# Kernel tuning notes

Hardware: AMD Instinct MI355X
Metric: run time of the kernel (lower is better)

Reference implementation:

```python
import jax, jax.numpy as jnp
import numpy as np

N_NODES = 50000
N_DIRECTED = 800000  # symmetrized to 1.6M (src,dst) pairs
IN_FEAT = 256
HEADS = 8
OUT = 64


def setup_inputs() -> dict:
    key = jax.random.key(0)
    k1, k2, k3, k4, k5 = jax.random.split(key, 5)
    r = jax.random.randint(k1, (N_DIRECTED,), 0, N_NODES)
    c = jax.random.randint(k2, (N_DIRECTED,), 0, N_NODES)
    # symmetric adjacency (values = 1), as edge list
    src = jnp.concatenate([r, c])
    dst = jnp.concatenate([c, r])
    x = jax.random.normal(k3, (N_NODES, IN_FEAT), dtype=jnp.float32)
    Ws = jax.random.normal(k4, (HEADS, OUT, IN_FEAT), dtype=jnp.float32) * 0.05
    As = jax.random.normal(k5, (HEADS, 2 * OUT, 1), dtype=jnp.float32) * 0.05
    return {"x": x, "src": src, "dst": dst, "Ws": Ws, "As": As}


def reference(x, src, dst, Ws, As):
    H, O, F = Ws.shape
    N = x.shape[0]
    # t_nodes = inputs @ Ws^T  -> [H, N, O]
    t = jnp.einsum('nf,hof->hno', x, Ws)
    a_l = As[:, :O, 0]   # [H, O]
    a_r = As[:, O:, 0]   # [H, O]
    Al = jnp.einsum('hno,ho->hn', t, a_l)  # [H, N]
    Ar = jnp.einsum('hno,ho->hn', t, a_r)  # [H, N]
    outs = []
    for k in range(H):
        # sparse E[i,j] = Al[i] + Ar[j] on adjacency pattern
        e = Al[k][src] + Ar[k][dst]  # [E]
        # NOTE: original applies tf.sparse.softmax to E directly (its lrelu
        # tensor is computed but never used), so no leaky_relu here.
        m = jax.ops.segment_max(e, src, num_segments=N)
        ex = jnp.exp(e - m[src])
        den = jax.ops.segment_sum(ex, src, num_segments=N)
        alpha = ex / den[src]
        # sparse_dense_matmul(alphas, t_nodes[k])
        h = jax.ops.segment_sum(alpha[:, None] * t[k][dst], src, num_segments=N)
        outs.append(h)
    out = jnp.stack(outs, axis=1)          # [N, H, O]
    out = out.reshape(N, H * O)            # reduction=False -> concat heads
    return jax.nn.elu(out)
```

## Files before the change

### kernel.cpp

```cpp
#include <hip/hip_runtime.h>
#include <hip/hip_bf16.h>

#define NN 50000
#define INF 256
#define NH 8
#define OUTF 64
#define NC 512
#define NGB 3128
#define EPB 8192
#define NBK 391
#define NBX 12501

typedef __attribute__((ext_vector_type(8))) short bf16x8;
typedef __attribute__((ext_vector_type(4))) float f32x4;
typedef __attribute__((ext_vector_type(2))) float v2f;
typedef __attribute__((ext_vector_type(8))) float f32x8;

__device__ __forceinline__ unsigned short f2bf(float f){
  unsigned u = __float_as_uint(f);
  u += 0x7FFFu + ((u>>16)&1u);
  return (unsigned short)(u>>16);
}

__global__ void k_atil(const float* __restrict__ W, const float* __restrict__ As,
                       float* __restrict__ atil, int* __restrict__ cursor){
  const int h = blockIdx.x, f = threadIdx.x;
  if (h==0 && f==0){ cursor[0]=0; cursor[1]=0; }
  float s = 0.f;
  for (int o=0;o<64;o++) s += W[((long)h*64+o)*INF + f] * As[h*128 + 64 + o];
  atil[h*256 + f] = s;
}

__global__ __launch_bounds__(256) void k_front(const float* __restrict__ x,
                                               const float* __restrict__ W,
                                               unsigned short* __restrict__ Wt,
                                               const float* __restrict__ atil,
                                               unsigned short* __restrict__ xb,
                                               float* __restrict__ eAr,
                                               const int* __restrict__ src,
                                               int* __restrict__ M,
                                               int E, int NB){
  __shared__ int hh[NBK];
  const int tid = threadIdx.x;
  const int bid = blockIdx.x;
  if (bid < 8){
    const int r = tid>>2, cb = (tid&3)*64;
    char* tile = (char*)(Wt + (size_t)bid*16384);
    const float* Wr = W + ((long)bid*64 + r)*INF;
#pragma unroll
    for (int i=0;i<16;i++){
      int c = cb + i*4;
      float4 v = *(const float4*)(Wr + c);
      ushort4 b; b.x=f2bf(v.x); b.y=f2bf(v.y); b.z=f2bf(v.z); b.w=f2bf(v.w);
      int addr = r*512 + ((((c>>3) ^ (r&7)))<<4) + ((c&7)<<1);
      *(ushort4*)(tile + addr) = b;
    }
    return;
  }
  if (bid < 8+NB){
    const int b = bid-8;
    for (int i=tid;i<NBK;i+=256) hh[i]=0;
    __syncthreads();
    const int base = b*EPB;
    const int lim = min(E-base, EPB);
    for (int i=tid;i<lim;i+=256) atomicAdd(&hh[src[base+i]>>7], 1);
    __syncthreads();
    for (int i=tid;i<NBK;i+=256) M[(long)i*NB + b] = hh[i];
    return;
  }
  const int w = tid>>6, l = tid&63;
  const long n = (long)(bid-8-NB)*4 + w;
  if (n > NN) return;
  if (n == NN){
    uint2 z; z.x=0; z.y=0;
    *(uint2*)((char*)xb + (size_t)n*512 + l*8) = z;
    if (l < 8) eAr[n*NH + l] = 0.f;
    return;
  }
  float4 v = *(const float4*)(x + n*INF + l*4);
  uint2 d;
  d.x = (unsigned)f2bf(v.x) | ((unsigned)f2bf(v.y)<<16);
  d.y = (unsigned)f2bf(v.z) | ((unsigned)f2bf(v.w)<<16);
  *(uint2*)((char*)xb + (size_t)n*512 + l*8) = d;
  float p[8];
#pragma unroll
  for (int h=0;h<8;h++){
    float4 a = *(const float4*)(atil + h*256 + l*4);
    p[h] = v.x*a.x + v.y*a.y + v.z*a.z + v.w*a.w;
  }
#pragma unroll
  for (int off=1; off<64; off<<=1){
#pragma unroll
    for (int h=0;h<8;h++) p[h] += __shfl_xor(p[h], off, 64);
  }
  if (l < 8){
    float e = p[0];
#pragma unroll
    for (int h=1;h<8;h++) if (l==h) e = p[h];
    eAr[n*NH + l] = __expf(e);
  }
}

__global__ __launch_bounds__(256) void k_bscan(int* __restrict__ M,
                                               int* __restrict__ bOff,
                                               int* __restrict__ bEnd,
                                               int* __restrict__ cursor, int NB){
  __shared__ int lds[256];
  __shared__ int sb;
  const int k = blockIdx.x, tid = threadIdx.x;
  int v = (tid<NB) ? M[(long)k*NB+tid] : 0;
  const int orig = v;
  lds[tid]=v; __syncthreads();
  for (int off=1; off<256; off<<=1){
    int a = (tid>=off)? lds[tid-off] : 0;
    __syncthreads(); lds[tid]+=a; __syncthreads();
  }
  if (tid==255){
    int tot = lds[255];
    int base = atomicAdd(&cursor[0], tot);
    sb = base;
    bOff[k] = base;
    bEnd[k] = base + tot;
  }
  __syncthreads();
  if (tid<NB) M[(long)k*NB+tid] = sb + lds[tid]-orig;
}

__global__ __launch_bounds__(256) void k_bscat(const int* __restrict__ src,
                                               const int* __restrict__ dst,
                                               const int* __restrict__ M,
                                               unsigned* __restrict__ ebuf,
                                               int E, int NB){
  __shared__ int cur[NBK];
  const int tid = threadIdx.x, b = blockIdx.x;
  for (int i=tid;i<NBK;i+=256) cur[i] = M[(long)i*NB + b];
  __syncthreads();
  const int base = b*EPB;
  const int lim = min(E-base, EPB);
  for (int i=tid;i<lim;i+=256){
    int s = src[base+i], d = dst[base+i];
    int p = atomicAdd(&cur[s>>7], 1);
    ebuf[p] = ((unsigned)d<<7) | (unsigned)(s&127);
  }
}

__global__ __launch_bounds__(256) void k_bcnt_final(const unsigned* __restrict__ ebuf,
                                                    const int* __restrict__ bOff,
                                                    const int* __restrict__ bEnd,
                                                    int* __restrict__ rbeg,
                                                    int* __restrict__ rend,
                                                    int* __restrict__ col,
                                                    int* __restrict__ cursor){
  __shared__ int h[128];
  __shared__ int s[128];
  __shared__ int cur[128];
  __shared__ int pend[128];
  __shared__ int sb;
  const int k = blockIdx.x, tid = threadIdx.x;
  if (tid<128) h[tid]=0;
  __syncthreads();
  const int beg = bOff[k], end = bEnd[k];
  for (int i=beg+tid; i<end; i+=256)
    atomicAdd(&h[(int)(ebuf[i] & 127u)], 1);
  __syncthreads();
  int pc = 0;
  if (tid<128){
    pc = (h[tid]+7)&~7;
    s[tid] = pc;
  }
  __syncthreads();
  for (int off=1; off<128; off<<=1){
    int a = (tid>=off && tid<128)? s[tid-off] : 0;
    __syncthreads();
    if (tid<128) s[tid] += a;
    __syncthreads();
  }
  if (tid==0){
    sb = atomicAdd(&cursor[1], s[127]);
  }
  __syncthreads();
  if (tid<128){
    int rp = sb + s[tid] - pc;
    rbeg[(k<<7)+tid] = rp;
    rend[(k<<7)+tid] = rp + pc;
    cur[tid] = rp;
    pend[tid] = rp + pc;
  }
  __syncthreads();
  for (int i=beg+tid; i<end; i+=256){
    unsigned e = ebuf[i];
    int p = atomicAdd(&cur[e & 127u], 1);
    col[p] = (int)(e>>7);
  }
  __syncthreads();
  if (tid<128){
    for (int i=cur[tid]; i<pend[tid]; i++) col[i] = NN;
  }
}

__global__ __launch_bounds__(512) void k_aggr_gemm(const int* __restrict__ rbeg,
                                                   const int* __restrict__ rend,
                                                   const int* __restrict__ col,
                                                   const unsigned short* __restrict__ xb,
                                                   const float* __restrict__ eAr,
                                                   const unsigned short* __restrict__ Wt,
                                                   float* __restrict__ out){
  __shared__ char gt[16*4096];
  __shared__ float sden[16][8];
  const int tid = threadIdx.x, l = tid&63, wid = tid>>6;
  const long nb = (long)blockIdx.x*16;
  const long l4 = (long)l*4;
  const int lw = l&7;

  for (int t=0; t<4; t++){
    const int task = wid*4 + t;
    const int r  = task>>1, fh = task&1;
    const long n = nb + r;
    const int beg = __builtin_amdgcn_readfirstlane(rbeg[n]);
    const int end = __builtin_amdgcn_readfirstlane(rend[n]);
    const char* xbp = (const char*)xb + fh*256;
    v2f acc[8] = {};
    float dnl = 0.f;
    for (int i=beg; i<end; i+=8){
      int cc[8];
#pragma unroll
      for (int e=0;e<8;e++) cc[e] = __builtin_amdgcn_readfirstlane(col[i+e]);
      unsigned q[8];
#pragma unroll
      for (int e=0;e<8;e++) q[e] = *(const unsigned*)(xbp + (size_t)cc[e]*512 + l4);
      float wl[8];
#pragma unroll
      for (int e=0;e<8;e++) wl[e] = eAr[(size_t)cc[e]*NH + lw];
#pragma unroll
      for (int e=0;e<8;e++) dnl += wl[e];
#pragma unroll
      for (int e=0;e<8;e++){
        f32x8 wv8 = *(const f32x8*)(eAr + (size_t)cc[e]*NH);
        v2f f01;
        f01.x = __uint_as_float(q[e]<<16);
        f01.y = __uint_as_float(q[e]&0xffff0000u);
#pragma unroll
        for (int h=0;h<8;h++){
          v2f w2; w2.x = wv8[h]; w2.y = wv8[h];
          acc[h] = __builtin_elementwise_fma(w2, f01, acc[h]);
        }
      }
    }
    char* seg = gt + r*4096;
    const int boff = (fh*256 + l*4) ^ ((r&7)<<4);
#pragma unroll
    for (int h=0;h<8;h++){
      unsigned d = (unsigned)f2bf(acc[h].x) | ((unsigned)f2bf(acc[h].y)<<16);
      *(unsigned*)(seg + h*512 + boff) = d;
    }
    if (fh==0 && l<8) sden[r][l] = dnl;
  }
  __syncthreads();

  const int h = wid;
  const char* Wh = (const char*)Wt + (size_t)h*32768;
  const int row = l&15;
  f32x4 acc2[4] = {};
  for (int ks=0; ks<8; ks++){
    const int ck = ks*4 + (l>>4);
    bf16x8 af = *(const bf16x8*)(gt + row*4096 + h*512 + ((ck ^ (row&7))<<4));
#pragma unroll
    for (int ct=0; ct<4; ct++){
      const int c = ct*16 + row;
      bf16x8 bfr = *(const bf16x8*)(Wh + c*512 + ((ck ^ (c&7))<<4));
      acc2[ct] = __builtin_amdgcn_mfma_f32_16x16x32_bf16(af, bfr, acc2[ct], 0,0,0);
    }
  }
  float lv[4];
#pragma unroll
  for (int j=0;j<4;j++){
    float dv = sden[(l>>4)*4 + j][h];
    lv[j] = dv>0.f ? 1.f/dv : 0.f;
  }
#pragma unroll
  for (int ct=0; ct<4; ct++){
#pragma unroll
    for (int j=0;j<4;j++){
      long gr = nb + (l>>4)*4 + j;
      if (gr < NN){
        float v = acc2[ct][j] * lv[j];
        out[gr*NC + h*64 + ct*16 + row] = v>0.f ? v : expm1f(v);
      }
    }
  }
}

extern "C" void kernel_launch(void* const* d_in, const int* in_sizes, int n_in,
                              void* d_out, int out_size, void* d_ws, size_t ws_size,
                              hipStream_t stream){
  const float* x   = (const float*)d_in[0];
  const int*   src = (const int*)d_in[1];
  const int*   dst = (const int*)d_in[2];
  const float* Ws  = (const float*)d_in[3];
  const float* Av  = (const float*)d_in[4];
  const int E = in_sizes[1];
  const int NB = (E + EPB - 1) / EPB;

  char* ws = (char*)d_ws;
  size_t off = 0;
  auto alloc = [&](size_t bytes)->void*{
    void* p = ws + off; off += (bytes + 255) & ~(size_t)255; return p;
  };
  unsigned short* xb   = (unsigned short*)alloc((size_t)50048*512);
  float* eAr           = (float*)alloc((size_t)50048*NH*4);
  float* atil          = (float*)alloc(8*256*4);
  unsigned short* Wt   = (unsigned short*)alloc((size_t)8*32768);
  int*   rbeg          = (int*)alloc(50304*4);
  int*   rend          = (int*)alloc(50304*4);
  int*   M             = (int*)alloc((size_t)NBK*256*4);
  int*   bOff          = (int*)alloc(512*4);
  int*   bEnd          = (int*)alloc(512*4);
  int*   cursor        = (int*)alloc(256);
  int*   col           = (int*)alloc(((size_t)E + 8*50048 + 64)*4);
  unsigned* ebuf       = (unsigned*)alloc((size_t)E*4);

  k_atil<<<8,256,0,stream>>>(Ws, Av, atil, cursor);
  k_front<<<8+NB+NBX,256,0,stream>>>(x, Ws, Wt, atil, xb, eAr, src, M, E, NB);
  k_bscan<<<NBK,256,0,stream>>>(M, bOff, bEnd, cursor, NB);
  k_bscat<<<NB,256,0,stream>>>(src, dst, M, ebuf, E, NB);
  k_bcnt_final<<<NBK,256,0,stream>>>(ebuf, bOff, bEnd, rbeg, rend, col, cursor);
  k_aggr_gemm<<<NGB,512,0,stream>>>(rbeg, rend, col, xb, eAr, Wt, (float*)d_out);
}
```

Before: 318.6 us.

## Use 1024-thread blocks with one wave per row and full-width gathers

The fused aggregate+GEMM kernel now launches 1024 threads, so each of the 16 waves gathers one whole destination row. Each lane loads 8 bytes (4 bf16 features) per neighbour instead of 4 bytes over two half-passes. The MFMA stage is split so each wave computes half of a head's output columns. This raises memory-level parallelism in the gather and removes the serial task loop, but doubles the accumulator registers per lane and relies on 1024-thread occupancy.

```diff
diff --git a/kernel.cpp b/kernel.cpp
--- a/kernel.cpp
+++ b/kernel.cpp
@@ -198,36 +198,35 @@
   }
 }
 
-__global__ __launch_bounds__(512) void k_aggr_gemm(const int* __restrict__ rbeg,
-                                                   const int* __restrict__ rend,
-                                                   const int* __restrict__ col,
-                                                   const unsigned short* __restrict__ xb,
-                                                   const float* __restrict__ eAr,
-                                                   const unsigned short* __restrict__ Wt,
-                                                   float* __restrict__ out){
+__global__ __launch_bounds__(1024) void k_aggr_gemm(const int* __restrict__ rbeg,
+                                                    const int* __restrict__ rend,
+                                                    const int* __restrict__ col,
+                                                    const unsigned short* __restrict__ xb,
+                                                    const float* __restrict__ eAr,
+                                                    const unsigned short* __restrict__ Wt,
+                                                    float* __restrict__ out){
   __shared__ char gt[16*4096];
   __shared__ float sden[16][8];
   const int tid = threadIdx.x, l = tid&63, wid = tid>>6;
   const long nb = (long)blockIdx.x*16;
-  const long l4 = (long)l*4;
+  const long l8 = (long)l*8;
   const int lw = l&7;
 
-  for (int t=0; t<4; t++){
-    const int task = wid*4 + t;
-    const int r  = task>>1, fh = task&1;
+  {
+    const int r = wid;
     const long n = nb + r;
     const int beg = __builtin_amdgcn_readfirstlane(rbeg[n]);
     const int end = __builtin_amdgcn_readfirstlane(rend[n]);
-    const char* xbp = (const char*)xb + fh*256;
-    v2f acc[8] = {};
+    const char* xbp = (const char*)xb;
+    v2f acc[8][2] = {};
     float dnl = 0.f;
     for (int i=beg; i<end; i+=8){
       int cc[8];
 #pragma unroll
       for (int e=0;e<8;e++) cc[e] = __builtin_amdgcn_readfirstlane(col[i+e]);
-      unsigned q[8];
-#pragma unroll
-      for (int e=0;e<8;e++) q[e] = *(const unsigned*)(xbp + (size_t)cc[e]*512 + l4);
+      uint2 q[8];
+#pragma unroll
+      for (int e=0;e<8;e++) q[e] = *(const uint2*)(xbp + (size_t)cc[e]*512 + l8);
       float wl[8];
 #pragma unroll
       for (int e=0;e<8;e++) wl[e] = eAr[(size_t)cc[e]*NH + lw];
@@ -236,37 +235,43 @@
 #pragma unroll
       for (int e=0;e<8;e++){
         f32x8 wv8 = *(const f32x8*)(eAr + (size_t)cc[e]*NH);
-        v2f f01;
-        f01.x = __uint_as_float(q[e]<<16);
-        f01.y = __uint_as_float(q[e]&0xffff0000u);
+        v2f f01, f23;
+        f01.x = __uint_as_float(q[e].x<<16);
+        f01.y = __uint_as_float(q[e].x&0xffff0000u);
+        f23.x = __uint_as_float(q[e].y<<16);
+        f23.y = __uint_as_float(q[e].y&0xffff0000u);
 #pragma unroll
         for (int h=0;h<8;h++){
           v2f w2; w2.x = wv8[h]; w2.y = wv8[h];
-          acc[h] = __builtin_elementwise_fma(w2, f01, acc[h]);
+          acc[h][0] = __builtin_elementwise_fma(w2, f01, acc[h][0]);
+          acc[h][1] = __builtin_elementwise_fma(w2, f23, acc[h][1]);
         }
       }
     }
     char* seg = gt + r*4096;
-    const int boff = (fh*256 + l*4) ^ ((r&7)<<4);
+    const int boff = (int)(l8 ^ ((r&7)<<4));
 #pragma unroll
     for (int h=0;h<8;h++){
-      unsigned d = (unsigned)f2bf(acc[h].x) | ((unsigned)f2bf(acc[h].y)<<16);
-      *(unsigned*)(seg + h*512 + boff) = d;
-    }
-    if (fh==0 && l<8) sden[r][l] = dnl;
-  }
-  __syncthreads();
-
-  const int h = wid;
+      uint2 d;
+      d.x = (unsigned)f2bf(acc[h][0].x) | ((unsigned)f2bf(acc[h][0].y)<<16);
+      d.y = (unsigned)f2bf(acc[h][1].x) | ((unsigned)f2bf(acc[h][1].y)<<16);
+      *(uint2*)(seg + h*512 + boff) = d;
+    }
+    if (l<8) sden[r][l] = dnl;
+  }
+  __syncthreads();
+
+  const int h = wid>>1;
+  const int chalf = wid&1;
   const char* Wh = (const char*)Wt + (size_t)h*32768;
   const int row = l&15;
-  f32x4 acc2[4] = {};
+  f32x4 acc2[2] = {};
   for (int ks=0; ks<8; ks++){
     const int ck = ks*4 + (l>>4);
     bf16x8 af = *(const bf16x8*)(gt + row*4096 + h*512 + ((ck ^ (row&7))<<4));
 #pragma unroll
-    for (int ct=0; ct<4; ct++){
-      const int c = ct*16 + row;
+    for (int ct=0; ct<2; ct++){
+      const int c = chalf*32 + ct*16 + row;
       bf16x8 bfr = *(const bf16x8*)(Wh + c*512 + ((ck ^ (c&7))<<4));
       acc2[ct] = __builtin_amdgcn_mfma_f32_16x16x32_bf16(af, bfr, acc2[ct], 0,0,0);
     }
@@ -278,13 +283,13 @@
     lv[j] = dv>0.f ? 1.f/dv : 0.f;
   }
 #pragma unroll
-  for (int ct=0; ct<4; ct++){
+  for (int ct=0; ct<2; ct++){
 #pragma unroll
     for (int j=0;j<4;j++){
       long gr = nb + (l>>4)*4 + j;
       if (gr < NN){
         float v = acc2[ct][j] * lv[j];
-        out[gr*NC + h*64 + ct*16 + row] = v>0.f ? v : expm1f(v);
+        out[gr*NC + h*64 + chalf*32 + ct*16 + row] = v>0.f ? v : expm1f(v);
       }
     }
   }
@@ -324,5 +329,5 @@
   k_bscan<<<NBK,256,0,stream>>>(M, bOff, bEnd, cursor, NB);
   k_bscat<<<NB,256,0,stream>>>(src, dst, M, ebuf, E, NB);
   k_bcnt_final<<<NBK,256,0,stream>>>(ebuf, bOff, bEnd, rbeg, rend, col, cursor);
-  k_aggr_gemm<<<NGB,512,0,stream>>>(rbeg, rend, col, xb, eAr, Wt, (float*)d_out);
-}
+  k_aggr_gemm<<<NGB,1024,0,stream>>>(rbeg, rend, col, xb, eAr, Wt, (float*)d_out);
+}
```

After: 287.9 us. -9.6%, faster.
